# Optimization experiments

Hardware: AMD Instinct MI355X
Metric: run time of the kernel (lower is better)

Reference implementation:

```python
import jax, jax.numpy as jnp
import numpy as np

N_NODES = 50000
N_EDGES = 800000
F_DIM = 64


def setup_inputs() -> dict:
    key = jax.random.key(0)
    ks = jax.random.split(key, 8)
    idx_i = jax.random.randint(ks[0], (N_EDGES,), 0, N_NODES)
    idx_j = jax.random.randint(ks[1], (N_EDGES,), 0, N_NODES)
    px = jax.random.normal(ks[2], (N_NODES, 3, F_DIM), dtype=jnp.float32)
    diff = jax.random.normal(ks[3], (N_EDGES, 3, 1), dtype=jnp.float32)
    s = 1.0 / np.sqrt(F_DIM)
    W_pp = jax.random.normal(ks[4], (F_DIM, F_DIM), dtype=jnp.float32) * s
    W_i = jax.random.normal(ks[5], (F_DIM, F_DIM), dtype=jnp.float32) * s
    W_j = jax.random.normal(ks[6], (F_DIM, F_DIM), dtype=jnp.float32) * s
    W_ii = jax.random.normal(ks[7], (F_DIM, F_DIM), dtype=jnp.float32) * s
    return {"idx_i": idx_i, "idx_j": idx_j, "px": px, "diff": diff,
            "W_pp": W_pp, "W_i": W_i, "W_j": W_j, "W_ii": W_ii}


def reference(idx_i, idx_j, px, diff, W_pp, W_i, W_j, W_ii):
    # PPLayer: bias-free linear on feature dim. px: [N, 3, F]
    px1 = jnp.einsum('nvf,gf->nvg', px, W_pp)
    # PIXLayer: gather endpoints, two bias-free linears, sum. [E, 3, F]
    ix = (jnp.einsum('evf,gf->evg', px1[idx_i], W_i)
          + jnp.einsum('evf,gf->evg', px1[idx_j], W_j))
    # ScaleLayer: elementwise scale by per-edge direction. diff: [E, 3, 1]
    ix = ix * diff
    # IILayer: bias-free linear on edge messages
    ix = jnp.einsum('evf,gf->evg', ix, W_ii)
    # IPLayer: scatter_add back to nodes along dim 0
    px_out = jax.ops.segment_sum(ix, idx_i, num_segments=N_NODES)
    return (px_out, ix)
```

## Files before the change

### kernel.cpp

```cpp
#include <hip/hip_runtime.h>

#define N_NODES 50000
#define N_EDGES 800000
#define F 64
#define NROWS (N_NODES * 3)
#define NPX (N_NODES * 3 * F)
#define NMM_BLOCKS ((NROWS + 63) / 64)
#define HIST_BLOCKS ((N_EDGES + 1023) / 1024)

typedef float floatx4 __attribute__((ext_vector_type(4)));
typedef unsigned short ushortx8 __attribute__((ext_vector_type(8)));

__device__ __forceinline__ unsigned short f2bf(float f) {
  unsigned int u = __float_as_uint(f);
  return (unsigned short)((u + 0x7FFFu + ((u >> 16) & 1u)) >> 16);
}
__device__ __forceinline__ float bf2f(unsigned short h) {
  return __uint_as_float(((unsigned int)h) << 16);
}

__global__ __launch_bounds__(256) void mm64_chain(
    const float* __restrict__ W_ii, const float* __restrict__ W_i,
    const float* __restrict__ W_j, const float* __restrict__ W_pp,
    float* __restrict__ Bi, float* __restrict__ Bj) {
  const float* Wx = (blockIdx.x == 0) ? W_i : W_j;
  float* Out = (blockIdx.x == 0) ? Bi : Bj;
  __shared__ float As[64][65];
  __shared__ float Bs[64][65];
  __shared__ float Ps[64][65];
  int t = threadIdx.x;
  for (int k = 0; k < 16; ++k) {
    int idx = t + 256 * k;
    As[idx >> 6][idx & 63] = W_ii[idx];
    Bs[idx >> 6][idx & 63] = Wx[idx];
    Ps[idx >> 6][idx & 63] = W_pp[idx];
  }
  __syncthreads();
  int g = t >> 2, f0 = (t & 3) * 16;
  float acc[16];
  #pragma unroll
  for (int j = 0; j < 16; ++j) acc[j] = 0.f;
  for (int k = 0; k < 64; ++k) {
    float a = As[g][k];
    #pragma unroll
    for (int j = 0; j < 16; ++j) acc[j] += a * Bs[k][f0 + j];
  }
  __syncthreads();
  #pragma unroll
  for (int j = 0; j < 16; ++j) As[g][f0 + j] = acc[j];
  __syncthreads();
  #pragma unroll
  for (int j = 0; j < 16; ++j) acc[j] = 0.f;
  for (int k = 0; k < 64; ++k) {
    float a = As[g][k];
    #pragma unroll
    for (int j = 0; j < 16; ++j) acc[j] += a * Ps[k][f0 + j];
  }
  for (int j = 0; j < 16; ++j) Out[g * 64 + f0 + j] = acc[j];
}

__global__ __launch_bounds__(256) void node_mm_hist(
    const float* __restrict__ px, const float* __restrict__ Bi,
    const float* __restrict__ Bj, float* __restrict__ yi,
    unsigned short* __restrict__ yjb,
    const int* __restrict__ idx_i, int* __restrict__ cnt) {
  __shared__ float pxs[64][68];
  __shared__ float Bs[128][68];
  if (blockIdx.x >= NMM_BLOCKS) {
    int b = blockIdx.x - NMM_BLOCKS;
    int base = b * 1024 + threadIdx.x;
    #pragma unroll
    for (int k = 0; k < 4; ++k) {
      int e = base + k * 256;
      if (e < N_EDGES) atomicAdd(&cnt[idx_i[e]], 1);
    }
    return;
  }
  int t = threadIdx.x;
  int r0 = blockIdx.x * 64;
  #pragma unroll
  for (int k = 0; k < 8; ++k) {
    int idx = t + 256 * k;
    int row = idx >> 4, c4 = (idx & 15) * 4;
    const float* src = (row < 64) ? (Bi + row * 64 + c4) : (Bj + (row - 64) * 64 + c4);
    *(float4*)&Bs[row][c4] = *(const float4*)src;
  }
  #pragma unroll
  for (int k = 0; k < 4; ++k) {
    int idx = t + 256 * k;
    int lr = idx >> 4, c4 = (idx & 15) * 4;
    float4 v = make_float4(0.f, 0.f, 0.f, 0.f);
    if (r0 + lr < NROWS) v = *(const float4*)(px + (size_t)(r0 + lr) * 64 + c4);
    *(float4*)&pxs[lr][c4] = v;
  }
  __syncthreads();
  int q = t & 31;
  int rg = t >> 5;
  float acc[8][4];
  #pragma unroll
  for (int r = 0; r < 8; ++r)
    #pragma unroll
    for (int j = 0; j < 4; ++j) acc[r][j] = 0.f;
  #pragma unroll 4
  for (int fc = 0; fc < 16; ++fc) {
    float4 b[4];
    #pragma unroll
    for (int j = 0; j < 4; ++j) b[j] = *(const float4*)&Bs[4 * q + j][fc * 4];
    #pragma unroll
    for (int r = 0; r < 8; ++r) {
      float4 p = *(const float4*)&pxs[rg * 8 + r][fc * 4];
      #pragma unroll
      for (int j = 0; j < 4; ++j)
        acc[r][j] += p.x * b[j].x + p.y * b[j].y + p.z * b[j].z + p.w * b[j].w;
    }
  }
  #pragma unroll
  for (int r = 0; r < 8; ++r) {
    int grow = r0 + rg * 8 + r;
    if (grow >= NROWS) continue;
    if (q < 16) {
      float4 v = make_float4(acc[r][0], acc[r][1], acc[r][2], acc[r][3]);
      *(float4*)(yi + (size_t)grow * 64 + q * 4) = v;
    } else {
      ushort4 h;
      h.x = f2bf(acc[r][0]); h.y = f2bf(acc[r][1]);
      h.z = f2bf(acc[r][2]); h.w = f2bf(acc[r][3]);
      *(ushort4*)(yjb + (size_t)grow * 64 + (q - 16) * 4) = h;
    }
  }
}

__global__ __launch_bounds__(1024) void scan_kernel(
    const int* __restrict__ cnt, int* __restrict__ offs, int* __restrict__ cursor) {
  __shared__ int wsum[16];
  __shared__ int s_carry;
  int t = threadIdx.x, w = t >> 6, l = t & 63;
  if (t == 0) { s_carry = 0; offs[0] = 0; }
  __syncthreads();
  for (int base = 0; base < N_NODES; base += 8192) {
    int i0 = base + t * 8;
    int x[8];
    if (i0 + 7 < N_NODES) {
      int4 a = *(const int4*)(cnt + i0);
      int4 b = *(const int4*)(cnt + i0 + 4);
      x[0] = a.x; x[1] = a.y; x[2] = a.z; x[3] = a.w;
      x[4] = b.x; x[5] = b.y; x[6] = b.z; x[7] = b.w;
    } else {
      #pragma unroll
      for (int k = 0; k < 8; ++k) x[k] = (i0 + k < N_NODES) ? cnt[i0 + k] : 0;
    }
    int incl[8];
    int p = 0;
    #pragma unroll
    for (int k = 0; k < 8; ++k) { p += x[k]; incl[k] = p; }
    int tsum = p;
    int ts = tsum;
    #pragma unroll
    for (int off = 1; off < 64; off <<= 1) {
      int y = __shfl_up(ts, off, 64);
      if (l >= off) ts += y;
    }
    if (l == 63) wsum[w] = ts;
    __syncthreads();
    if (t < 16) {
      int ws_ = wsum[t];
      int si = ws_;
      #pragma unroll
      for (int off = 1; off < 16; off <<= 1) {
        int y = __shfl_up(si, off, 16);
        if (t >= off) si += y;
      }
      wsum[t] = si - ws_;
    }
    __syncthreads();
    int basev = s_carry + wsum[w] + (ts - tsum);
    #pragma unroll
    for (int k = 0; k < 8; ++k) {
      int i = i0 + k;
      if (i < N_NODES) {
        int it = basev + incl[k];
        offs[i + 1] = it;
        cursor[i] = it - x[k];
      }
    }
    __syncthreads();
    if (t == 1023) s_carry = basev + tsum;
    __syncthreads();
  }
}

__global__ __launch_bounds__(256) void scatter_kernel(
    const int* __restrict__ idx_i, const int* __restrict__ idx_j,
    const float* __restrict__ diff, int* __restrict__ cursor,
    int* __restrict__ perm, int* __restrict__ pnj, float* __restrict__ pdiff) {
  int e = blockIdx.x * 256 + threadIdx.x;
  if (e < N_EDGES) {
    int pos = atomicAdd(&cursor[idx_i[e]], 1);
    perm[pos] = e;
    pnj[pos] = idx_j[e];
    pdiff[pos * 3 + 0] = diff[e * 3 + 0];
    pdiff[pos * 3 + 1] = diff[e * 3 + 1];
    pdiff[pos * 3 + 2] = diff[e * 3 + 2];
  }
}

__global__ __launch_bounds__(192) void node_edge_kernel(
    const int* __restrict__ offs, const int* __restrict__ perm,
    const int* __restrict__ pnj, const float* __restrict__ pdiff,
    const float* __restrict__ yi, const unsigned short* __restrict__ yjb,
    float* __restrict__ ix_out, float* __restrict__ px_out) {
  int n = blockIdx.x;
  int v = threadIdx.x >> 6;
  int lane = threadIdx.x & 63;
  int s = lane >> 3;
  int fo = (lane & 7) * 8;
  int start = offs[n], end = offs[n + 1];
  size_t nrow = ((size_t)n * 3 + v) * 64 + fo;
  const floatx4 yia = __builtin_nontemporal_load((const floatx4*)(yi + nrow));
  const floatx4 yib = __builtin_nontemporal_load((const floatx4*)(yi + nrow + 4));
  float yi8[8] = {yia.x, yia.y, yia.z, yia.w, yib.x, yib.y, yib.z, yib.w};
  float pacc[8];
  #pragma unroll
  for (int j = 0; j < 8; ++j) pacc[j] = 0.f;

  for (int p = start + s; p < end; p += 8) {
    int e   = perm[p];
    int nj  = pnj[p];
    float d = pdiff[p * 3 + v];
    const ushortx8 yw = *(const ushortx8*)(yjb + ((size_t)nj * 3 + v) * 64 + fo);
    float r[8];
    #pragma unroll
    for (int j = 0; j < 8; ++j) {
      float yjv = bf2f(yw[j]);
      r[j] = d * (yi8[j] + yjv);
      pacc[j] += r[j];
    }
    float* dst = ix_out + ((size_t)e * 3 + v) * 64 + fo;
    floatx4 r0 = {r[0], r[1], r[2], r[3]};
    floatx4 r1 = {r[4], r[5], r[6], r[7]};
    __builtin_nontemporal_store(r0, (floatx4*)dst);
    __builtin_nontemporal_store(r1, (floatx4*)(dst + 4));
  }
  #pragma unroll
  for (int m = 8; m < 64; m <<= 1) {
    #pragma unroll
    for (int j = 0; j < 8; ++j) pacc[j] += __shfl_xor(pacc[j], m, 64);
  }
  if (s == 0) {
    floatx4 o0 = {pacc[0], pacc[1], pacc[2], pacc[3]};
    floatx4 o1 = {pacc[4], pacc[5], pacc[6], pacc[7]};
    __builtin_nontemporal_store(o0, (floatx4*)(px_out + nrow));
    __builtin_nontemporal_store(o1, (floatx4*)(px_out + nrow + 4));
  }
}

extern "C" void kernel_launch(void* const* d_in, const int* in_sizes, int n_in,
                              void* d_out, int out_size, void* d_ws, size_t ws_size,
                              hipStream_t stream) {
  const int*   idx_i = (const int*)d_in[0];
  const int*   idx_j = (const int*)d_in[1];
  const float* px    = (const float*)d_in[2];
  const float* diff  = (const float*)d_in[3];
  const float* W_pp  = (const float*)d_in[4];
  const float* W_i   = (const float*)d_in[5];
  const float* W_j   = (const float*)d_in[6];
  const float* W_ii  = (const float*)d_in[7];

  float* px_out = (float*)d_out;
  float* ix_out = (float*)d_out + NPX;

  float* ws = (float*)d_ws;
  float* yi = ws;
  unsigned short* yjb = (unsigned short*)(yi + (size_t)NPX);
  float* Bi = (float*)(yjb + (size_t)NPX);
  float* Bj = Bi + 4096;
  int* cnt    = (int*)(Bj + 4096);
  int* offs   = cnt + N_NODES;
  int* cursor = offs + N_NODES + 1;
  int* perm   = cursor + N_NODES;
  int* pnj    = perm + N_EDGES;
  float* pdiff = (float*)(pnj + N_EDGES);

  (void)hipMemsetAsync(cnt, 0, N_NODES * sizeof(int), stream);

  mm64_chain<<<2, 256, 0, stream>>>(W_ii, W_i, W_j, W_pp, Bi, Bj);

  node_mm_hist<<<NMM_BLOCKS + HIST_BLOCKS, 256, 0, stream>>>(
      px, Bi, Bj, yi, yjb, idx_i, cnt);

  scan_kernel<<<1, 1024, 0, stream>>>(cnt, offs, cursor);
  scatter_kernel<<<(N_EDGES + 255) / 256, 256, 0, stream>>>(
      idx_i, idx_j, diff, cursor, perm, pnj, pdiff);

  node_edge_kernel<<<N_NODES, 192, 0, stream>>>(offs, perm, pnj, pdiff,
                                                yi, yjb, ix_out, px_out);
}
```

Measured before the change: 363.3 us.

## Stream ix in edge order and accumulate px via factored yi·sum(d)

```diff
diff --git a/kernel.cpp b/kernel.cpp
--- a/kernel.cpp
+++ b/kernel.cpp
@@ -4,6 +4,7 @@
 #define N_EDGES 800000
 #define F 64
 #define NROWS (N_NODES * 3)
+#define EROWS (N_EDGES * 3)
 #define NPX (N_NODES * 3 * F)
 #define NMM_BLOCKS ((NROWS + 63) / 64)
 #define HIST_BLOCKS ((N_EDGES + 1023) / 1024)
@@ -61,8 +62,8 @@
 
 __global__ __launch_bounds__(256) void node_mm_hist(
     const float* __restrict__ px, const float* __restrict__ Bi,
-    const float* __restrict__ Bj, float* __restrict__ yi,
-    unsigned short* __restrict__ yjb,
+    const float* __restrict__ Bj, unsigned short* __restrict__ ybi,
+    unsigned short* __restrict__ ybj,
     const int* __restrict__ idx_i, int* __restrict__ cnt) {
   __shared__ float pxs[64][68];
   __shared__ float Bs[128][68];
@@ -118,15 +119,11 @@
   for (int r = 0; r < 8; ++r) {
     int grow = r0 + rg * 8 + r;
     if (grow >= NROWS) continue;
-    if (q < 16) {
-      float4 v = make_float4(acc[r][0], acc[r][1], acc[r][2], acc[r][3]);
-      *(float4*)(yi + (size_t)grow * 64 + q * 4) = v;
-    } else {
-      ushort4 h;
-      h.x = f2bf(acc[r][0]); h.y = f2bf(acc[r][1]);
-      h.z = f2bf(acc[r][2]); h.w = f2bf(acc[r][3]);
-      *(ushort4*)(yjb + (size_t)grow * 64 + (q - 16) * 4) = h;
-    }
+    ushort4 h;
+    h.x = f2bf(acc[r][0]); h.y = f2bf(acc[r][1]);
+    h.z = f2bf(acc[r][2]); h.w = f2bf(acc[r][3]);
+    if (q < 16) *(ushort4*)(ybi + (size_t)grow * 64 + q * 4) = h;
+    else        *(ushort4*)(ybj + (size_t)grow * 64 + (q - 16) * 4) = h;
   }
 }
 
@@ -189,68 +186,79 @@
   }
 }
 
-__global__ __launch_bounds__(256) void scatter_kernel(
+__global__ __launch_bounds__(256) void edge_stream_kernel(
     const int* __restrict__ idx_i, const int* __restrict__ idx_j,
-    const float* __restrict__ diff, int* __restrict__ cursor,
-    int* __restrict__ perm, int* __restrict__ pnj, float* __restrict__ pdiff) {
-  int e = blockIdx.x * 256 + threadIdx.x;
-  if (e < N_EDGES) {
-    int pos = atomicAdd(&cursor[idx_i[e]], 1);
-    perm[pos] = e;
-    pnj[pos] = idx_j[e];
-    pdiff[pos * 3 + 0] = diff[e * 3 + 0];
-    pdiff[pos * 3 + 1] = diff[e * 3 + 1];
-    pdiff[pos * 3 + 2] = diff[e * 3 + 2];
-  }
-}
-
-__global__ __launch_bounds__(192) void node_edge_kernel(
-    const int* __restrict__ offs, const int* __restrict__ perm,
-    const int* __restrict__ pnj, const float* __restrict__ pdiff,
-    const float* __restrict__ yi, const unsigned short* __restrict__ yjb,
-    float* __restrict__ ix_out, float* __restrict__ px_out) {
+    const float* __restrict__ diff,
+    const unsigned short* __restrict__ ybi, const unsigned short* __restrict__ ybj,
+    float* __restrict__ ix_out,
+    int* __restrict__ cursor, int* __restrict__ pnj, float* __restrict__ pdiff) {
+  unsigned int gid = blockIdx.x * 256 + threadIdx.x;
+  int row = gid >> 3;
+  int e = row / 3;
+  int v = row - e * 3;
+  int fo = (gid & 7) * 8;
+  int ni = idx_i[e];
+  int nj = idx_j[e];
+  float d = diff[row];
+  const ushortx8 a = *(const ushortx8*)(ybi + ((size_t)ni * 3 + v) * 64 + fo);
+  const ushortx8 b = *(const ushortx8*)(ybj + ((size_t)nj * 3 + v) * 64 + fo);
+  floatx4 r0, r1;
+  r0.x = d * (bf2f(a[0]) + bf2f(b[0]));
+  r0.y = d * (bf2f(a[1]) + bf2f(b[1]));
+  r0.z = d * (bf2f(a[2]) + bf2f(b[2]));
+  r0.w = d * (bf2f(a[3]) + bf2f(b[3]));
+  r1.x = d * (bf2f(a[4]) + bf2f(b[4]));
+  r1.y = d * (bf2f(a[5]) + bf2f(b[5]));
+  r1.z = d * (bf2f(a[6]) + bf2f(b[6]));
+  r1.w = d * (bf2f(a[7]) + bf2f(b[7]));
+  float* dst = ix_out + (size_t)row * 64 + fo;
+  __builtin_nontemporal_store(r0, (floatx4*)dst);
+  __builtin_nontemporal_store(r1, (floatx4*)(dst + 4));
+  if (((gid & 7) == 0) && (v == 0)) {
+    int pos = atomicAdd(&cursor[ni], 1);
+    pnj[pos] = nj;
+    pdiff[pos * 3 + 0] = d;
+    pdiff[pos * 3 + 1] = diff[row + 1];
+    pdiff[pos * 3 + 2] = diff[row + 2];
+  }
+}
+
+__global__ __launch_bounds__(192) void node_accum_kernel(
+    const int* __restrict__ offs, const int* __restrict__ pnj,
+    const float* __restrict__ pdiff,
+    const unsigned short* __restrict__ ybi, const unsigned short* __restrict__ ybj,
+    float* __restrict__ px_out) {
   int n = blockIdx.x;
   int v = threadIdx.x >> 6;
   int lane = threadIdx.x & 63;
-  int s = lane >> 3;
-  int fo = (lane & 7) * 8;
+  int s = lane >> 4;
+  int fq = (lane & 15) * 4;
   int start = offs[n], end = offs[n + 1];
-  size_t nrow = ((size_t)n * 3 + v) * 64 + fo;
-  const floatx4 yia = __builtin_nontemporal_load((const floatx4*)(yi + nrow));
-  const floatx4 yib = __builtin_nontemporal_load((const floatx4*)(yi + nrow + 4));
-  float yi8[8] = {yia.x, yia.y, yia.z, yia.w, yib.x, yib.y, yib.z, yib.w};
-  float pacc[8];
-  #pragma unroll
-  for (int j = 0; j < 8; ++j) pacc[j] = 0.f;
-
-  for (int p = start + s; p < end; p += 8) {
-    int e   = perm[p];
+  const ushort4 yw = *(const ushort4*)(ybi + ((size_t)n * 3 + v) * 64 + fq);
+  float4 yiv = make_float4(bf2f(yw.x), bf2f(yw.y), bf2f(yw.z), bf2f(yw.w));
+  float4 acc = make_float4(0.f, 0.f, 0.f, 0.f);
+  float sum_d = 0.f;
+
+  for (int p = start + s; p < end; p += 4) {
     int nj  = pnj[p];
     float d = pdiff[p * 3 + v];
-    const ushortx8 yw = *(const ushortx8*)(yjb + ((size_t)nj * 3 + v) * 64 + fo);
-    float r[8];
-    #pragma unroll
-    for (int j = 0; j < 8; ++j) {
-      float yjv = bf2f(yw[j]);
-      r[j] = d * (yi8[j] + yjv);
-      pacc[j] += r[j];
-    }
-    float* dst = ix_out + ((size_t)e * 3 + v) * 64 + fo;
-    floatx4 r0 = {r[0], r[1], r[2], r[3]};
-    floatx4 r1 = {r[4], r[5], r[6], r[7]};
-    __builtin_nontemporal_store(r0, (floatx4*)dst);
-    __builtin_nontemporal_store(r1, (floatx4*)(dst + 4));
-  }
-  #pragma unroll
-  for (int m = 8; m < 64; m <<= 1) {
-    #pragma unroll
-    for (int j = 0; j < 8; ++j) pacc[j] += __shfl_xor(pacc[j], m, 64);
+    const ushort4 w = *(const ushort4*)(ybj + ((size_t)nj * 3 + v) * 64 + fq);
+    acc.x += d * bf2f(w.x); acc.y += d * bf2f(w.y);
+    acc.z += d * bf2f(w.z); acc.w += d * bf2f(w.w);
+    sum_d += d;
+  }
+  #pragma unroll
+  for (int mm = 16; mm < 64; mm <<= 1) {
+    acc.x += __shfl_xor(acc.x, mm, 64);
+    acc.y += __shfl_xor(acc.y, mm, 64);
+    acc.z += __shfl_xor(acc.z, mm, 64);
+    acc.w += __shfl_xor(acc.w, mm, 64);
+    sum_d += __shfl_xor(sum_d, mm, 64);
   }
   if (s == 0) {
-    floatx4 o0 = {pacc[0], pacc[1], pacc[2], pacc[3]};
-    floatx4 o1 = {pacc[4], pacc[5], pacc[6], pacc[7]};
-    __builtin_nontemporal_store(o0, (floatx4*)(px_out + nrow));
-    __builtin_nontemporal_store(o1, (floatx4*)(px_out + nrow + 4));
+    float4 o = make_float4(yiv.x * sum_d + acc.x, yiv.y * sum_d + acc.y,
+                           yiv.z * sum_d + acc.z, yiv.w * sum_d + acc.w);
+    *(float4*)(px_out + ((size_t)n * 3 + v) * 64 + fq) = o;
   }
 }
 
@@ -269,16 +277,14 @@
   float* px_out = (float*)d_out;
   float* ix_out = (float*)d_out + NPX;
 
-  float* ws = (float*)d_ws;
-  float* yi = ws;
-  unsigned short* yjb = (unsigned short*)(yi + (size_t)NPX);
-  float* Bi = (float*)(yjb + (size_t)NPX);
+  unsigned short* ybi = (unsigned short*)d_ws;
+  unsigned short* ybj = ybi + (size_t)NPX;
+  float* Bi = (float*)(ybj + (size_t)NPX);
   float* Bj = Bi + 4096;
   int* cnt    = (int*)(Bj + 4096);
   int* offs   = cnt + N_NODES;
   int* cursor = offs + N_NODES + 1;
-  int* perm   = cursor + N_NODES;
-  int* pnj    = perm + N_EDGES;
+  int* pnj    = cursor + N_NODES;
   float* pdiff = (float*)(pnj + N_EDGES);
 
   (void)hipMemsetAsync(cnt, 0, N_NODES * sizeof(int), stream);
@@ -286,12 +292,13 @@
   mm64_chain<<<2, 256, 0, stream>>>(W_ii, W_i, W_j, W_pp, Bi, Bj);
 
   node_mm_hist<<<NMM_BLOCKS + HIST_BLOCKS, 256, 0, stream>>>(
-      px, Bi, Bj, yi, yjb, idx_i, cnt);
+      px, Bi, Bj, ybi, ybj, idx_i, cnt);
 
   scan_kernel<<<1, 1024, 0, stream>>>(cnt, offs, cursor);
-  scatter_kernel<<<(N_EDGES + 255) / 256, 256, 0, stream>>>(
-      idx_i, idx_j, diff, cursor, perm, pnj, pdiff);
-
-  node_edge_kernel<<<N_NODES, 192, 0, stream>>>(offs, perm, pnj, pdiff,
-                                                yi, yjb, ix_out, px_out);
-}
+
+  edge_stream_kernel<<<(EROWS * 8) / 256, 256, 0, stream>>>(
+      idx_i, idx_j, diff, ybi, ybj, ix_out, cursor, pnj, pdiff);
+
+  node_accum_kernel<<<N_NODES, 192, 0, stream>>>(offs, pnj, pdiff,
+                                                 ybi, ybj, px_out);
+}
```

After: 418.2 us. 15.1% more time.
